# Kernel optimization log

Measured on AMD Instinct MI355X. Metric: run time of the kernel, lower is better.

Reference implementation:

```python
import jax, jax.numpy as jnp
import numpy as np


def setup_inputs() -> dict:
    key = jax.random.key(0)
    k1, k2, k3 = jax.random.split(key, 3)
    N, E, D_IN, D_OUT = 100000, 1600000, 64, 64
    x = jax.random.normal(k1, (N, D_IN), dtype=jnp.float32)
    edge_index = jax.random.randint(k2, (2, E), 0, N, dtype=jnp.int64)
    # Glorot-style init for the GCN weight, zero bias (PyG defaults)
    W = jax.random.normal(k3, (D_IN, D_OUT), dtype=jnp.float32) * (1.0 / np.sqrt(D_IN))
    b = jnp.zeros((D_OUT,), dtype=jnp.float32)
    return {"x": x, "edge_index": edge_index, "W": W, "b": b}


def reference(x, edge_index, W, b):
    # GCNConv (PyG semantics, add_self_loops=True, normalize=True) followed by
    # Dropout (eval mode -> identity) and ReLU.
    N = x.shape[0]
    # Linear transform first (small GEMM)
    xw = x @ W  # [N, D_OUT]
    # Add self-loops
    loops = jnp.arange(N, dtype=edge_index.dtype)
    row = jnp.concatenate([edge_index[0], loops])  # source nodes
    col = jnp.concatenate([edge_index[1], loops])  # destination nodes
    # Symmetric degree normalization: deg over destination index (PyG gcn_norm)
    ones = jnp.ones(col.shape[0], dtype=xw.dtype)
    deg = jax.ops.segment_sum(ones, col, num_segments=N)
    deg_inv_sqrt = jnp.where(deg > 0, jax.lax.rsqrt(deg), 0.0)
    norm = deg_inv_sqrt[row] * deg_inv_sqrt[col]  # [E+N]
    # Gather source features, scale, scatter-add to destinations
    msgs = norm[:, None] * xw[row]  # [E+N, D_OUT]
    out = jax.ops.segment_sum(msgs, col, num_segments=N)
    out = out + b
    # dropout in eval mode is identity
    return jax.nn.relu(out)
```

## Files before the change

### kernel.cpp

```cpp
#include <hip/hip_runtime.h>
#include <hip/hip_fp16.h>


#define D 64
#define BW 256
#define CAP 6144
#define EPT 16
#define PART_T 256
#define EPB (PART_T * EPT)

typedef __attribute__((ext_vector_type(8))) short bf16x8;
typedef __attribute__((ext_vector_type(4))) float f32x4;

__device__ __forceinline__ unsigned short f2bf(float f) {
    unsigned u = __float_as_uint(f);
    u += 0x7FFFu + ((u >> 16) & 1u);
    return (unsigned short)(u >> 16);
}

__global__ void k_part(const int* __restrict__ row, const int* __restrict__ col,
                       int* __restrict__ gcur, int* __restrict__ packed,
                       int E, int NBUCK) {
    extern __shared__ int sh[];
    int* lh   = sh;
    int* base = sh + NBUCK;
    for (int i = threadIdx.x; i < NBUCK; i += PART_T) lh[i] = 0;
    __syncthreads();
    int e0 = blockIdx.x * EPB + threadIdx.x;
    int rr[EPT], cc[EPT], pp[EPT];
#pragma unroll
    for (int i = 0; i < EPT; ++i) {
        int e = e0 + i * PART_T;
        if (e < E) {
            cc[i] = col[e];
            rr[i] = row[e];
            pp[i] = atomicAdd(&lh[cc[i] >> 8], 1);
        } else {
            cc[i] = -1;
        }
    }
    __syncthreads();
    int rot = (int)((blockIdx.x * 97u) % (unsigned)NBUCK);
    for (int j = threadIdx.x; j < NBUCK; j += PART_T) {
        int bu = j + rot; if (bu >= NBUCK) bu -= NBUCK;
        int h = lh[bu];
        if (h > 0) base[bu] = atomicAdd(&gcur[bu * 32], h);
    }
    __syncthreads();
#pragma unroll
    for (int i = 0; i < EPT; ++i) {
        if (cc[i] >= 0) {
            int bu = cc[i] >> 8;
            int pos = base[bu] + pp[i];
            if (pos < CAP)
                packed[(size_t)bu * CAP + pos] = (rr[i] << 8) | (cc[i] & 255);
        }
    }
}

__global__ void k_dis(const int* __restrict__ gcur, const int* __restrict__ packed,
                      float* __restrict__ dis, int N) {
    __shared__ int lh[BW];
    int b = blockIdx.x;
    lh[threadIdx.x] = 0;
    __syncthreads();
    int sz = min(gcur[b * 32], CAP);
    const int* pk = packed + (size_t)b * CAP;
    for (int i = threadIdx.x; i < sz; i += BW)
        atomicAdd(&lh[pk[i] & 255], 1);
    __syncthreads();
    int n = b * BW + threadIdx.x;
    if (n < N) dis[n] = rsqrtf((float)(lh[threadIdx.x] + 1));
}

__global__ __launch_bounds__(256, 4)
void k_gemm_mfma(const float* __restrict__ x, const float* __restrict__ W,
                 const float* __restrict__ dis, unsigned short* __restrict__ xw_h,
                 int N) {
    __shared__ float Ws[64 * 64];
    int tid = threadIdx.x;
    for (int i = tid; i < 4096; i += 256) Ws[i] = W[i];
    __syncthreads();
    int lane = tid & 63, wv = tid >> 6;
    int m = lane & 15, quad = lane >> 4;
    bf16x8 Bf[4][2];
#pragma unroll
    for (int t = 0; t < 4; ++t)
#pragma unroll
        for (int s = 0; s < 2; ++s) {
            bf16x8 f;
#pragma unroll
            for (int j = 0; j < 8; ++j)
                f[j] = (short)f2bf(Ws[(s * 32 + quad * 8 + j) * 64 + t * 16 + m]);
            Bf[t][s] = f;
        }
    int mt = blockIdx.x * 4 + wv;
    int row0 = mt * 16;
    if (row0 >= N) return;
    const float* xr = x + (size_t)(row0 + m) * 64 + quad * 8;
    float4 a0 = *(const float4*)(xr);
    float4 a1 = *(const float4*)(xr + 4);
    float4 a2 = *(const float4*)(xr + 32);
    float4 a3 = *(const float4*)(xr + 36);
    bf16x8 A0, A1;
    A0[0] = (short)f2bf(a0.x); A0[1] = (short)f2bf(a0.y);
    A0[2] = (short)f2bf(a0.z); A0[3] = (short)f2bf(a0.w);
    A0[4] = (short)f2bf(a1.x); A0[5] = (short)f2bf(a1.y);
    A0[6] = (short)f2bf(a1.z); A0[7] = (short)f2bf(a1.w);
    A1[0] = (short)f2bf(a2.x); A1[1] = (short)f2bf(a2.y);
    A1[2] = (short)f2bf(a2.z); A1[3] = (short)f2bf(a2.w);
    A1[4] = (short)f2bf(a3.x); A1[5] = (short)f2bf(a3.y);
    A1[6] = (short)f2bf(a3.z); A1[7] = (short)f2bf(a3.w);
    f32x4 acc[4];
#pragma unroll
    for (int t = 0; t < 4; ++t) {
        acc[t] = (f32x4){0.f, 0.f, 0.f, 0.f};
        acc[t] = __builtin_amdgcn_mfma_f32_16x16x32_bf16(A0, Bf[t][0], acc[t], 0, 0, 0);
        acc[t] = __builtin_amdgcn_mfma_f32_16x16x32_bf16(A1, Bf[t][1], acc[t], 0, 0, 0);
    }
    float4 dv = *(const float4*)(dis + row0 + quad * 4);
    float dsc[4] = {dv.x, dv.y, dv.z, dv.w};
#pragma unroll
    for (int t = 0; t < 4; ++t)
#pragma unroll
        for (int r = 0; r < 4; ++r) {
            int grow = row0 + quad * 4 + r;
            int gcol = t * 16 + m;
            xw_h[(size_t)grow * 64 + gcol] =
                __half_as_ushort(__float2half(acc[t][r] * dsc[r]));
        }
}

__global__ __launch_bounds__(1024, 8)
void k_gather(const int* __restrict__ gcur, const int* __restrict__ packed,
              const uint2* __restrict__ xwh, const float* __restrict__ bias,
              float4* __restrict__ out4, int N) {
    __shared__ int lh[BW], stt[BW], cur[BW];
    __shared__ int srtL[CAP];
    __shared__ int wsum[4];
    int b = blockIdx.x;
    int tid = threadIdx.x;
    if (tid < BW) lh[tid] = 0;
    __syncthreads();
    int sz = min(gcur[b * 32], CAP);
    const int* pk = packed + (size_t)b * CAP;
    for (int i = tid; i < sz; i += 1024)
        atomicAdd(&lh[pk[i] & 255], 1);
    __syncthreads();
    int lane = tid & 63, wv4 = tid >> 6;
    int v = (tid < BW) ? lh[tid] : 0;
    int s = v;
#pragma unroll
    for (int off = 1; off < 64; off <<= 1) {
        int u = __shfl_up(s, off);
        if (lane >= off) s += u;
    }
    if (tid < BW && lane == 63) wsum[wv4] = s;
    __syncthreads();
    if (tid < BW) {
        int woff = 0;
        for (int w = 0; w < 4; ++w) woff += (w < wv4) ? wsum[w] : 0;
        int st = woff + s - v;
        stt[tid] = st;
        cur[tid] = st;
    }
    __syncthreads();
    for (int i = tid; i < sz; i += 1024) {
        int p = pk[i];
        int pos = atomicAdd(&cur[p & 255], 1);
        srtL[pos] = p >> 8;
    }
    __syncthreads();
    int wv = tid >> 6;
    int q = lane >> 4;
    int l = lane & 15;
    const float4 bb = ((const float4*)bias)[l];
#define ADDV(h)                                                     \
    {                                                               \
        __half2 h0 = *(__half2*)&(h).x, h1 = *(__half2*)&(h).y;     \
        float2 f0 = __half22float2(h0), f1 = __half22float2(h1);    \
        acc.x += f0.x; acc.y += f0.y; acc.z += f1.x; acc.w += f1.y; \
    }
    for (int nn = wv * 16; nn < wv * 16 + 16; ++nn) {
        int node = b * BW + nn;
        if (node >= N) break;
        int k = lh[nn], s0 = stt[nn];
        float4 acc = make_float4(0.f, 0.f, 0.f, 0.f);
        if (q == 0) { uint2 hs = xwh[(size_t)node * 16 + l]; ADDV(hs); }
        int j = q;
        for (; j + 12 < k; j += 16) {
            int r0 = srtL[s0 + j];
            int r1 = srtL[s0 + j + 4];
            int r2 = srtL[s0 + j + 8];
            int r3 = srtL[s0 + j + 12];
            uint2 va = xwh[(size_t)r0 * 16 + l];
            uint2 vb = xwh[(size_t)r1 * 16 + l];
            uint2 vc = xwh[(size_t)r2 * 16 + l];
            uint2 vd = xwh[(size_t)r3 * 16 + l];
            ADDV(va); ADDV(vb); ADDV(vc); ADDV(vd);
        }
        for (; j < k; j += 4) { uint2 ve = xwh[(size_t)srtL[s0 + j] * 16 + l]; ADDV(ve); }
#pragma unroll
        for (int mm = 16; mm < 64; mm <<= 1) {
            acc.x += __shfl_xor(acc.x, mm);
            acc.y += __shfl_xor(acc.y, mm);
            acc.z += __shfl_xor(acc.z, mm);
            acc.w += __shfl_xor(acc.w, mm);
        }
        if (q == 0) {
            float dn = rsqrtf((float)(k + 1));
            float4 o;
            o.x = fmaxf(fmaf(dn, acc.x, bb.x), 0.f);
            o.y = fmaxf(fmaf(dn, acc.y, bb.y), 0.f);
            o.z = fmaxf(fmaf(dn, acc.z, bb.z), 0.f);
            o.w = fmaxf(fmaf(dn, acc.w, bb.w), 0.f);
            out4[(size_t)node * 16 + l] = o;
        }
    }
#undef ADDV
}

extern "C" void kernel_launch(void* const* d_in, const int* in_sizes, int n_in,
                              void* d_out, int out_size, void* d_ws, size_t ws_size,
                              hipStream_t stream) {
    const float* x    = (const float*)d_in[0];
    const int*   ei   = (const int*)d_in[1];
    const float* W    = (const float*)d_in[2];
    const float* bias = (const float*)d_in[3];
    float* out = (float*)d_out;

    const int N = in_sizes[0] / D;
    const int E = in_sizes[1] / 2;
    const int* row = ei;
    const int* col = ei + E;

    const int NBUCK = (N + BW - 1) / BW;
    const int NB1   = (E + EPB - 1) / EPB;
    const int NT    = (N + 15) / 16;

    char* ws = (char*)d_ws;
    size_t off = 0;
    unsigned short* xw_h = (unsigned short*)(ws + off); off += (size_t)N * D * sizeof(unsigned short);
    int* packed   = (int*)(ws + off);     off += (size_t)NBUCK * CAP * sizeof(int);
    int* gcur     = (int*)(ws + off);     off += (size_t)NBUCK * 32 * sizeof(int);
    float* dis    = (float*)(ws + off);   off += (size_t)N * sizeof(float);

    size_t ldsPart = 2u * (size_t)NBUCK * sizeof(int);

    hipMemsetAsync(gcur, 0, (size_t)NBUCK * 32 * sizeof(int), stream);
    k_part<<<NB1, PART_T, ldsPart, stream>>>(row, col, gcur, packed, E, NBUCK);
    k_dis<<<NBUCK, BW, 0, stream>>>(gcur, packed, dis, N);
    k_gemm_mfma<<<(NT + 3) / 4, 256, 0, stream>>>(x, W, dis, xw_h, N);
    k_gather<<<NBUCK, 1024, 0, stream>>>(gcur, packed, (const uint2*)xw_h, bias,
                                         (float4*)out, N);
}
```

Before: 160.9 us.

## Fuse partition, degree and gather into one cooperative kernel with grid syncs

Merges the edge partitioning, degree computation and gather-aggregate stages into a single cooperative kernel of 256 persistent blocks separated by grid-wide syncs. Bucket contents are held in registers between phases, which removes the second global read of packed edges. The gcur memset is folded into the GEMM kernel. The source-side normalization moves from the GEMM epilogue into the gather as a per-edge dis lookup, so the GEMM no longer has to wait for degrees. The cost is an extra scattered load per edge, grid.sync overhead, and parallelism fixed at 256 blocks with two buckets each. It also assumes edge and bucket counts fit the fixed per-thread register arrays.

```diff
diff --git a/kernel.cpp b/kernel.cpp
--- a/kernel.cpp
+++ b/kernel.cpp
@@ -1,13 +1,18 @@
 #include <hip/hip_runtime.h>
 #include <hip/hip_fp16.h>
+#include <hip/hip_cooperative_groups.h>
+
+namespace cg = cooperative_groups;
 
 
 #define D 64
 #define BW 256
+#define MAXB 512
 #define CAP 6144
-#define EPT 16
-#define PART_T 256
-#define EPB (PART_T * EPT)
+#define RPT 6
+#define GRID 256
+#define BT 1024
+#define EPT 7
 
 typedef __attribute__((ext_vector_type(8))) short bf16x8;
 typedef __attribute__((ext_vector_type(4))) float f32x4;
@@ -18,65 +23,12 @@
     return (unsigned short)(u >> 16);
 }
 
-__global__ void k_part(const int* __restrict__ row, const int* __restrict__ col,
-                       int* __restrict__ gcur, int* __restrict__ packed,
-                       int E, int NBUCK) {
-    extern __shared__ int sh[];
-    int* lh   = sh;
-    int* base = sh + NBUCK;
-    for (int i = threadIdx.x; i < NBUCK; i += PART_T) lh[i] = 0;
-    __syncthreads();
-    int e0 = blockIdx.x * EPB + threadIdx.x;
-    int rr[EPT], cc[EPT], pp[EPT];
-#pragma unroll
-    for (int i = 0; i < EPT; ++i) {
-        int e = e0 + i * PART_T;
-        if (e < E) {
-            cc[i] = col[e];
-            rr[i] = row[e];
-            pp[i] = atomicAdd(&lh[cc[i] >> 8], 1);
-        } else {
-            cc[i] = -1;
-        }
-    }
-    __syncthreads();
-    int rot = (int)((blockIdx.x * 97u) % (unsigned)NBUCK);
-    for (int j = threadIdx.x; j < NBUCK; j += PART_T) {
-        int bu = j + rot; if (bu >= NBUCK) bu -= NBUCK;
-        int h = lh[bu];
-        if (h > 0) base[bu] = atomicAdd(&gcur[bu * 32], h);
-    }
-    __syncthreads();
-#pragma unroll
-    for (int i = 0; i < EPT; ++i) {
-        if (cc[i] >= 0) {
-            int bu = cc[i] >> 8;
-            int pos = base[bu] + pp[i];
-            if (pos < CAP)
-                packed[(size_t)bu * CAP + pos] = (rr[i] << 8) | (cc[i] & 255);
-        }
-    }
-}
-
-__global__ void k_dis(const int* __restrict__ gcur, const int* __restrict__ packed,
-                      float* __restrict__ dis, int N) {
-    __shared__ int lh[BW];
-    int b = blockIdx.x;
-    lh[threadIdx.x] = 0;
-    __syncthreads();
-    int sz = min(gcur[b * 32], CAP);
-    const int* pk = packed + (size_t)b * CAP;
-    for (int i = threadIdx.x; i < sz; i += BW)
-        atomicAdd(&lh[pk[i] & 255], 1);
-    __syncthreads();
-    int n = b * BW + threadIdx.x;
-    if (n < N) dis[n] = rsqrtf((float)(lh[threadIdx.x] + 1));
-}
-
 __global__ __launch_bounds__(256, 4)
-void k_gemm_mfma(const float* __restrict__ x, const float* __restrict__ W,
-                 const float* __restrict__ dis, unsigned short* __restrict__ xw_h,
-                 int N) {
+void k_gemm(const float* __restrict__ x, const float* __restrict__ W,
+            unsigned short* __restrict__ xw_h, int* __restrict__ zero_base,
+            int nzero, int N) {
+    int zi = blockIdx.x * 256 + threadIdx.x;
+    if (zi < nzero) zero_base[zi] = 0;
     __shared__ float Ws[64 * 64];
     int tid = threadIdx.x;
     for (int i = tid; i < 4096; i += 256) Ws[i] = W[i];
@@ -118,8 +70,6 @@
         acc[t] = __builtin_amdgcn_mfma_f32_16x16x32_bf16(A0, Bf[t][0], acc[t], 0, 0, 0);
         acc[t] = __builtin_amdgcn_mfma_f32_16x16x32_bf16(A1, Bf[t][1], acc[t], 0, 0, 0);
     }
-    float4 dv = *(const float4*)(dis + row0 + quad * 4);
-    float dsc[4] = {dv.x, dv.y, dv.z, dv.w};
 #pragma unroll
     for (int t = 0; t < 4; ++t)
 #pragma unroll
@@ -127,97 +77,172 @@
             int grow = row0 + quad * 4 + r;
             int gcol = t * 16 + m;
             xw_h[(size_t)grow * 64 + gcol] =
-                __half_as_ushort(__float2half(acc[t][r] * dsc[r]));
-        }
-}
-
-__global__ __launch_bounds__(1024, 8)
-void k_gather(const int* __restrict__ gcur, const int* __restrict__ packed,
-              const uint2* __restrict__ xwh, const float* __restrict__ bias,
-              float4* __restrict__ out4, int N) {
-    __shared__ int lh[BW], stt[BW], cur[BW];
+                __half_as_ushort(__float2half(acc[t][r]));
+        }
+}
+
+__global__ __launch_bounds__(BT, 4)
+void k_fused(const int* __restrict__ row, const int* __restrict__ col,
+             int* __restrict__ gcur, int* __restrict__ packed,
+             float* __restrict__ disg, const uint2* __restrict__ xwh,
+             const float* __restrict__ bias, float4* __restrict__ out4,
+             int E, int N, int NBUCK) {
+    __shared__ int lhp[MAXB];
+    __shared__ int basep[MAXB];
+    __shared__ int lhb[2][BW];
+    __shared__ int stt[BW], cur[BW];
+    __shared__ int wsum[4];
     __shared__ int srtL[CAP];
-    __shared__ int wsum[4];
-    int b = blockIdx.x;
+
+    cg::grid_group grid = cg::this_grid();
     int tid = threadIdx.x;
-    if (tid < BW) lh[tid] = 0;
-    __syncthreads();
-    int sz = min(gcur[b * 32], CAP);
-    const int* pk = packed + (size_t)b * CAP;
-    for (int i = tid; i < sz; i += 1024)
-        atomicAdd(&lh[pk[i] & 255], 1);
-    __syncthreads();
-    int lane = tid & 63, wv4 = tid >> 6;
-    int v = (tid < BW) ? lh[tid] : 0;
-    int s = v;
-#pragma unroll
-    for (int off = 1; off < 64; off <<= 1) {
-        int u = __shfl_up(s, off);
-        if (lane >= off) s += u;
-    }
-    if (tid < BW && lane == 63) wsum[wv4] = s;
-    __syncthreads();
-    if (tid < BW) {
-        int woff = 0;
-        for (int w = 0; w < 4; ++w) woff += (w < wv4) ? wsum[w] : 0;
-        int st = woff + s - v;
-        stt[tid] = st;
-        cur[tid] = st;
-    }
-    __syncthreads();
-    for (int i = tid; i < sz; i += 1024) {
-        int p = pk[i];
-        int pos = atomicAdd(&cur[p & 255], 1);
-        srtL[pos] = p >> 8;
-    }
-    __syncthreads();
-    int wv = tid >> 6;
+    int bk  = (int)blockIdx.x;
+
+    for (int i = tid; i < NBUCK; i += BT) lhp[i] = 0;
+    __syncthreads();
+    int epb = (E + GRID - 1) / GRID;
+    int e0 = bk * epb;
+    int eend = min(e0 + epb, E);
+    int rr[EPT], cc[EPT], pp[EPT];
+#pragma unroll
+    for (int i = 0; i < EPT; ++i) {
+        int e = e0 + i * BT + tid;
+        if (e < eend) {
+            cc[i] = col[e]; rr[i] = row[e];
+            pp[i] = atomicAdd(&lhp[cc[i] >> 8], 1);
+        } else cc[i] = -1;
+    }
+    __syncthreads();
+    int rot = (int)((bk * 97u) % (unsigned)NBUCK);
+    for (int j = tid; j < NBUCK; j += BT) {
+        int bu = j + rot; if (bu >= NBUCK) bu -= NBUCK;
+        int h = lhp[bu];
+        if (h > 0) basep[bu] = atomicAdd(&gcur[bu * 32], h);
+    }
+    __syncthreads();
+#pragma unroll
+    for (int i = 0; i < EPT; ++i) {
+        if (cc[i] >= 0) {
+            int bu = cc[i] >> 8;
+            int pos = basep[bu] + pp[i];
+            if (pos < CAP)
+                packed[(size_t)bu * CAP + pos] = (rr[i] << 8) | (cc[i] & 255);
+        }
+    }
+    grid.sync();
+
+    int rv[2][RPT];
+#pragma unroll
+    for (int p = 0; p < 2; ++p) {
+        int b = bk + p * GRID;
+        if (b < NBUCK) {
+            if (tid < BW) lhb[p][tid] = 0;
+            __syncthreads();
+            int sz = min(gcur[b * 32], CAP);
+            const int* pk = packed + (size_t)b * CAP;
+#pragma unroll
+            for (int i = 0; i < RPT; ++i) {
+                int idx = i * BT + tid;
+                int v = (idx < sz) ? pk[idx] : -1;
+                rv[p][i] = v;
+                if (v >= 0) atomicAdd(&lhb[p][v & 255], 1);
+            }
+            __syncthreads();
+            if (tid < BW) {
+                int n = b * BW + tid;
+                if (n < N) disg[n] = rsqrtf((float)(lhb[p][tid] + 1));
+            }
+        }
+    }
+    grid.sync();
+
+    int lane = tid & 63, wv = tid >> 6;
     int q = lane >> 4;
     int l = lane & 15;
     const float4 bb = ((const float4*)bias)[l];
-#define ADDV(h)                                                     \
-    {                                                               \
-        __half2 h0 = *(__half2*)&(h).x, h1 = *(__half2*)&(h).y;     \
-        float2 f0 = __half22float2(h0), f1 = __half22float2(h1);    \
-        acc.x += f0.x; acc.y += f0.y; acc.z += f1.x; acc.w += f1.y; \
-    }
-    for (int nn = wv * 16; nn < wv * 16 + 16; ++nn) {
-        int node = b * BW + nn;
-        if (node >= N) break;
-        int k = lh[nn], s0 = stt[nn];
-        float4 acc = make_float4(0.f, 0.f, 0.f, 0.f);
-        if (q == 0) { uint2 hs = xwh[(size_t)node * 16 + l]; ADDV(hs); }
-        int j = q;
-        for (; j + 12 < k; j += 16) {
-            int r0 = srtL[s0 + j];
-            int r1 = srtL[s0 + j + 4];
-            int r2 = srtL[s0 + j + 8];
-            int r3 = srtL[s0 + j + 12];
-            uint2 va = xwh[(size_t)r0 * 16 + l];
-            uint2 vb = xwh[(size_t)r1 * 16 + l];
-            uint2 vc = xwh[(size_t)r2 * 16 + l];
-            uint2 vd = xwh[(size_t)r3 * 16 + l];
-            ADDV(va); ADDV(vb); ADDV(vc); ADDV(vd);
-        }
-        for (; j < k; j += 4) { uint2 ve = xwh[(size_t)srtL[s0 + j] * 16 + l]; ADDV(ve); }
-#pragma unroll
-        for (int mm = 16; mm < 64; mm <<= 1) {
-            acc.x += __shfl_xor(acc.x, mm);
-            acc.y += __shfl_xor(acc.y, mm);
-            acc.z += __shfl_xor(acc.z, mm);
-            acc.w += __shfl_xor(acc.w, mm);
-        }
-        if (q == 0) {
+#define ADDS(h, ww)                                                         \
+    {                                                                       \
+        __half2 h0 = *(__half2*)&(h).x, h1 = *(__half2*)&(h).y;             \
+        float2 f0 = __half22float2(h0), f1 = __half22float2(h1);            \
+        acc.x = fmaf((ww), f0.x, acc.x); acc.y = fmaf((ww), f0.y, acc.y);   \
+        acc.z = fmaf((ww), f1.x, acc.z); acc.w = fmaf((ww), f1.y, acc.w);   \
+    }
+    for (int p = 0; p < 2; ++p) {
+        int b = bk + p * GRID;
+        if (b >= NBUCK) break;
+        __syncthreads();
+        int v = (tid < BW) ? lhb[p][tid] : 0;
+        int s = v;
+#pragma unroll
+        for (int off = 1; off < 64; off <<= 1) {
+            int u = __shfl_up(s, off);
+            if (lane >= off) s += u;
+        }
+        if (tid < BW && lane == 63) wsum[wv] = s;
+        __syncthreads();
+        if (tid < BW) {
+            int woff = 0;
+            for (int w = 0; w < 4; ++w) woff += (w < wv) ? wsum[w] : 0;
+            int st = woff + s - v;
+            stt[tid] = st; cur[tid] = st;
+        }
+        __syncthreads();
+#pragma unroll
+        for (int i = 0; i < RPT; ++i) {
+            int pv = rv[p][i];
+            if (pv >= 0) {
+                int pos = atomicAdd(&cur[pv & 255], 1);
+                srtL[pos] = pv >> 8;
+            }
+        }
+        __syncthreads();
+        for (int nn = wv * 16; nn < wv * 16 + 16; ++nn) {
+            int node = b * BW + nn;
+            if (node >= N) break;
+            int k = lhb[p][nn], s0 = stt[nn];
             float dn = rsqrtf((float)(k + 1));
-            float4 o;
-            o.x = fmaxf(fmaf(dn, acc.x, bb.x), 0.f);
-            o.y = fmaxf(fmaf(dn, acc.y, bb.y), 0.f);
-            o.z = fmaxf(fmaf(dn, acc.z, bb.z), 0.f);
-            o.w = fmaxf(fmaf(dn, acc.w, bb.w), 0.f);
-            out4[(size_t)node * 16 + l] = o;
-        }
-    }
-#undef ADDV
+            float4 acc = make_float4(0.f, 0.f, 0.f, 0.f);
+            if (q == 0) {
+                uint2 hs = xwh[(size_t)node * 16 + l];
+                ADDS(hs, dn);
+            }
+            int j = q;
+            for (; j + 12 < k; j += 16) {
+                int r0 = srtL[s0 + j];
+                int r1 = srtL[s0 + j + 4];
+                int r2 = srtL[s0 + j + 8];
+                int r3 = srtL[s0 + j + 12];
+                float w0 = disg[r0], w1 = disg[r1], w2 = disg[r2], w3 = disg[r3];
+                uint2 va = xwh[(size_t)r0 * 16 + l];
+                uint2 vb = xwh[(size_t)r1 * 16 + l];
+                uint2 vc = xwh[(size_t)r2 * 16 + l];
+                uint2 vd = xwh[(size_t)r3 * 16 + l];
+                ADDS(va, w0); ADDS(vb, w1); ADDS(vc, w2); ADDS(vd, w3);
+            }
+            for (; j < k; j += 4) {
+                int r = srtL[s0 + j];
+                float wr = disg[r];
+                uint2 ve = xwh[(size_t)r * 16 + l];
+                ADDS(ve, wr);
+            }
+#pragma unroll
+            for (int mm = 16; mm < 64; mm <<= 1) {
+                acc.x += __shfl_xor(acc.x, mm);
+                acc.y += __shfl_xor(acc.y, mm);
+                acc.z += __shfl_xor(acc.z, mm);
+                acc.w += __shfl_xor(acc.w, mm);
+            }
+            if (q == 0) {
+                float4 o;
+                o.x = fmaxf(fmaf(dn, acc.x, bb.x), 0.f);
+                o.y = fmaxf(fmaf(dn, acc.y, bb.y), 0.f);
+                o.z = fmaxf(fmaf(dn, acc.z, bb.z), 0.f);
+                o.w = fmaxf(fmaf(dn, acc.w, bb.w), 0.f);
+                out4[(size_t)node * 16 + l] = o;
+            }
+        }
+    }
+#undef ADDS
 }
 
 extern "C" void kernel_launch(void* const* d_in, const int* in_sizes, int n_in,
@@ -229,28 +254,30 @@
     const float* bias = (const float*)d_in[3];
     float* out = (float*)d_out;
 
-    const int N = in_sizes[0] / D;
-    const int E = in_sizes[1] / 2;
-    const int* row = ei;
-    const int* col = ei + E;
-
-    const int NBUCK = (N + BW - 1) / BW;
-    const int NB1   = (E + EPB - 1) / EPB;
-    const int NT    = (N + 15) / 16;
+    int N = in_sizes[0] / D;
+    int E = in_sizes[1] / 2;
+    const int* rowp = ei;
+    const int* colp = ei + E;
+
+    int NBUCK = (N + BW - 1) / BW;
+    const int NT = (N + 15) / 16;
 
     char* ws = (char*)d_ws;
     size_t off = 0;
-    unsigned short* xw_h = (unsigned short*)(ws + off); off += (size_t)N * D * sizeof(unsigned short);
-    int* packed   = (int*)(ws + off);     off += (size_t)NBUCK * CAP * sizeof(int);
-    int* gcur     = (int*)(ws + off);     off += (size_t)NBUCK * 32 * sizeof(int);
-    float* dis    = (float*)(ws + off);   off += (size_t)N * sizeof(float);
-
-    size_t ldsPart = 2u * (size_t)NBUCK * sizeof(int);
-
-    hipMemsetAsync(gcur, 0, (size_t)NBUCK * 32 * sizeof(int), stream);
-    k_part<<<NB1, PART_T, ldsPart, stream>>>(row, col, gcur, packed, E, NBUCK);
-    k_dis<<<NBUCK, BW, 0, stream>>>(gcur, packed, dis, N);
-    k_gemm_mfma<<<(NT + 3) / 4, 256, 0, stream>>>(x, W, dis, xw_h, N);
-    k_gather<<<NBUCK, 1024, 0, stream>>>(gcur, packed, (const uint2*)xw_h, bias,
-                                         (float4*)out, N);
-}
+    unsigned short* xw_h = (unsigned short*)(ws + off);
+    off += (size_t)N * D * sizeof(unsigned short);
+    int* packed = (int*)(ws + off); off += (size_t)NBUCK * CAP * sizeof(int);
+    int* gcur   = (int*)(ws + off); off += (size_t)NBUCK * 32 * sizeof(int);
+    float* disg = (float*)(ws + off); off += (size_t)N * sizeof(float);
+
+    int nzero = NBUCK * 32;
+
+    k_gemm<<<(NT + 3) / 4, 256, 0, stream>>>(x, W, xw_h, gcur, nzero, N);
+
+    const uint2* xwh_c = (const uint2*)xw_h;
+    float4* outp = (float4*)out;
+    void* args[] = {(void*)&rowp, (void*)&colp, (void*)&gcur, (void*)&packed,
+                    (void*)&disg, (void*)&xwh_c, (void*)&bias, (void*)&outp,
+                    (void*)&E, (void*)&N, (void*)&NBUCK};
+    (void)hipLaunchCooperativeKernel((void*)k_fused, dim3(GRID), dim3(BT), args, 0, stream);
+}
```

New measurement: 261.6 us. 1.63x slower.

## Replace atomic bucket partition with histogram-scan counting sort; move source norm to gather

Applied to the files above, without the earlier changes.

The single-pass partition that grabbed bucket offsets with global atomics into fixed-capacity slabs is replaced by a two-pass counting sort. A per-block bucket histogram is followed by a three-kernel exclusive scan and a scatter into a compact packed array, so bucket ranges are contiguous and deterministic. The GEMM no longer scales rows by the source degree norm and can run first. The gather instead loads the per-source norm for every edge and uses FMAs. This removes global atomic contention and the CAP-strided layout, at the cost of more kernel launches, an extra read of col, and one extra scalar gather per edge.

```diff
diff --git a/kernel.cpp b/kernel.cpp
--- a/kernel.cpp
+++ b/kernel.cpp
@@ -5,9 +5,9 @@
 #define D 64
 #define BW 256
 #define CAP 6144
-#define EPT 16
 #define PART_T 256
-#define EPB (PART_T * EPT)
+#define EPB 4096
+#define SCAN_CHUNK 1024
 
 typedef __attribute__((ext_vector_type(8))) short bf16x8;
 typedef __attribute__((ext_vector_type(4))) float f32x4;
@@ -18,65 +18,9 @@
     return (unsigned short)(u >> 16);
 }
 
-__global__ void k_part(const int* __restrict__ row, const int* __restrict__ col,
-                       int* __restrict__ gcur, int* __restrict__ packed,
-                       int E, int NBUCK) {
-    extern __shared__ int sh[];
-    int* lh   = sh;
-    int* base = sh + NBUCK;
-    for (int i = threadIdx.x; i < NBUCK; i += PART_T) lh[i] = 0;
-    __syncthreads();
-    int e0 = blockIdx.x * EPB + threadIdx.x;
-    int rr[EPT], cc[EPT], pp[EPT];
-#pragma unroll
-    for (int i = 0; i < EPT; ++i) {
-        int e = e0 + i * PART_T;
-        if (e < E) {
-            cc[i] = col[e];
-            rr[i] = row[e];
-            pp[i] = atomicAdd(&lh[cc[i] >> 8], 1);
-        } else {
-            cc[i] = -1;
-        }
-    }
-    __syncthreads();
-    int rot = (int)((blockIdx.x * 97u) % (unsigned)NBUCK);
-    for (int j = threadIdx.x; j < NBUCK; j += PART_T) {
-        int bu = j + rot; if (bu >= NBUCK) bu -= NBUCK;
-        int h = lh[bu];
-        if (h > 0) base[bu] = atomicAdd(&gcur[bu * 32], h);
-    }
-    __syncthreads();
-#pragma unroll
-    for (int i = 0; i < EPT; ++i) {
-        if (cc[i] >= 0) {
-            int bu = cc[i] >> 8;
-            int pos = base[bu] + pp[i];
-            if (pos < CAP)
-                packed[(size_t)bu * CAP + pos] = (rr[i] << 8) | (cc[i] & 255);
-        }
-    }
-}
-
-__global__ void k_dis(const int* __restrict__ gcur, const int* __restrict__ packed,
-                      float* __restrict__ dis, int N) {
-    __shared__ int lh[BW];
-    int b = blockIdx.x;
-    lh[threadIdx.x] = 0;
-    __syncthreads();
-    int sz = min(gcur[b * 32], CAP);
-    const int* pk = packed + (size_t)b * CAP;
-    for (int i = threadIdx.x; i < sz; i += BW)
-        atomicAdd(&lh[pk[i] & 255], 1);
-    __syncthreads();
-    int n = b * BW + threadIdx.x;
-    if (n < N) dis[n] = rsqrtf((float)(lh[threadIdx.x] + 1));
-}
-
 __global__ __launch_bounds__(256, 4)
-void k_gemm_mfma(const float* __restrict__ x, const float* __restrict__ W,
-                 const float* __restrict__ dis, unsigned short* __restrict__ xw_h,
-                 int N) {
+void k_gemm(const float* __restrict__ x, const float* __restrict__ W,
+            unsigned short* __restrict__ xw_h, int N) {
     __shared__ float Ws[64 * 64];
     int tid = threadIdx.x;
     for (int i = tid; i < 4096; i += 256) Ws[i] = W[i];
@@ -94,8 +38,7 @@
                 f[j] = (short)f2bf(Ws[(s * 32 + quad * 8 + j) * 64 + t * 16 + m]);
             Bf[t][s] = f;
         }
-    int mt = blockIdx.x * 4 + wv;
-    int row0 = mt * 16;
+    int row0 = (blockIdx.x * 4 + wv) * 16;
     if (row0 >= N) return;
     const float* xr = x + (size_t)(row0 + m) * 64 + quad * 8;
     float4 a0 = *(const float4*)(xr);
@@ -118,23 +61,131 @@
         acc[t] = __builtin_amdgcn_mfma_f32_16x16x32_bf16(A0, Bf[t][0], acc[t], 0, 0, 0);
         acc[t] = __builtin_amdgcn_mfma_f32_16x16x32_bf16(A1, Bf[t][1], acc[t], 0, 0, 0);
     }
-    float4 dv = *(const float4*)(dis + row0 + quad * 4);
-    float dsc[4] = {dv.x, dv.y, dv.z, dv.w};
 #pragma unroll
     for (int t = 0; t < 4; ++t)
 #pragma unroll
-        for (int r = 0; r < 4; ++r) {
-            int grow = row0 + quad * 4 + r;
-            int gcol = t * 16 + m;
-            xw_h[(size_t)grow * 64 + gcol] =
-                __half_as_ushort(__float2half(acc[t][r] * dsc[r]));
-        }
+        for (int r = 0; r < 4; ++r)
+            xw_h[(size_t)(row0 + quad * 4 + r) * 64 + t * 16 + m] =
+                __half_as_ushort(__float2half(acc[t][r]));
+}
+
+__global__ void k_hist1(const int* __restrict__ col, int* __restrict__ hist,
+                        int E, int NB1, int NBUCK) {
+    extern __shared__ int lhist[];
+    int bk = blockIdx.x;
+    for (int bu = threadIdx.x; bu < NBUCK; bu += PART_T) lhist[bu] = 0;
+    __syncthreads();
+    int base = bk * EPB;
+#pragma unroll 4
+    for (int i = threadIdx.x; i < EPB; i += PART_T) {
+        int e = base + i;
+        if (e < E) atomicAdd(&lhist[col[e] >> 8], 1);
+    }
+    __syncthreads();
+    for (int bu = threadIdx.x; bu < NBUCK; bu += PART_T)
+        hist[bu * NB1 + bk] = lhist[bu];
+}
+
+__global__ void k_blocksum(const int* __restrict__ src, int* __restrict__ partial, int L) {
+    int base = blockIdx.x * SCAN_CHUNK;
+    int s = 0;
+    for (int i = threadIdx.x; i < SCAN_CHUNK; i += 256) {
+        int idx = base + i;
+        s += (idx < L) ? src[idx] : 0;
+    }
+#pragma unroll
+    for (int off = 32; off > 0; off >>= 1) s += __shfl_down(s, off);
+    __shared__ int ws[4];
+    if ((threadIdx.x & 63) == 0) ws[threadIdx.x >> 6] = s;
+    __syncthreads();
+    if (threadIdx.x == 0) partial[blockIdx.x] = ws[0] + ws[1] + ws[2] + ws[3];
+}
+
+__global__ void k_scan_partials(int* __restrict__ partial, int P) {
+    __shared__ int wtot[4];
+    int i = threadIdx.x;
+    int v = (i < P) ? partial[i] : 0;
+    int lane = i & 63, wv = i >> 6;
+    int s = v;
+#pragma unroll
+    for (int off = 1; off < 64; off <<= 1) {
+        int t = __shfl_up(s, off);
+        if (lane >= off) s += t;
+    }
+    if (lane == 63) wtot[wv] = s;
+    __syncthreads();
+    int woff = 0;
+    for (int w = 0; w < 4; ++w) woff += (w < wv) ? wtot[w] : 0;
+    if (i < P) partial[i] = woff + s - v;
+}
+
+__global__ void k_scan_excl(const int* __restrict__ src, const int* __restrict__ partial,
+                            int* __restrict__ dst, int L) {
+    __shared__ int wsum[4];
+    int lane = threadIdx.x & 63, wv = threadIdx.x >> 6;
+    int base = blockIdx.x * SCAN_CHUNK + threadIdx.x * 4;
+    int v0 = (base + 0 < L) ? src[base + 0] : 0;
+    int v1 = (base + 1 < L) ? src[base + 1] : 0;
+    int v2 = (base + 2 < L) ? src[base + 2] : 0;
+    int v3 = (base + 3 < L) ? src[base + 3] : 0;
+    int t = v0 + v1 + v2 + v3;
+    int s = t;
+#pragma unroll
+    for (int off = 1; off < 64; off <<= 1) {
+        int u = __shfl_up(s, off);
+        if (lane >= off) s += u;
+    }
+    if (lane == 63) wsum[wv] = s;
+    __syncthreads();
+    int woff = 0;
+    for (int w = 0; w < 4; ++w) woff += (w < wv) ? wsum[w] : 0;
+    int excl = partial[blockIdx.x] + woff + (s - t);
+    if (base + 0 < L) dst[base + 0] = excl;
+    if (base + 1 < L) dst[base + 1] = excl + v0;
+    if (base + 2 < L) dst[base + 2] = excl + v0 + v1;
+    if (base + 3 < L) dst[base + 3] = excl + v0 + v1 + v2;
+}
+
+__global__ void k_scatter1(const int* __restrict__ row, const int* __restrict__ col,
+                           const int* __restrict__ histS, int* __restrict__ packed,
+                           int E, int NB1, int NBUCK) {
+    extern __shared__ int cur[];
+    int bk = blockIdx.x;
+    for (int bu = threadIdx.x; bu < NBUCK; bu += PART_T)
+        cur[bu] = histS[bu * NB1 + bk];
+    __syncthreads();
+    int base = bk * EPB;
+#pragma unroll 4
+    for (int i = threadIdx.x; i < EPB; i += PART_T) {
+        int e = base + i;
+        if (e < E) {
+            int c = col[e], r = row[e];
+            int pos = atomicAdd(&cur[c >> 8], 1);
+            packed[pos] = (r << 8) | (c & 255);
+        }
+    }
+}
+
+__global__ void k_dis(const int* __restrict__ histS, const int* __restrict__ packed,
+                      float* __restrict__ disg, int E, int NB1, int NBUCK, int N) {
+    __shared__ int lh[BW];
+    int b = blockIdx.x;
+    int lo = histS[b * NB1];
+    int hi = (b == NBUCK - 1) ? E : histS[(b + 1) * NB1];
+    lh[threadIdx.x] = 0;
+    __syncthreads();
+    for (int i = lo + threadIdx.x; i < hi; i += BW)
+        atomicAdd(&lh[packed[i] & 255], 1);
+    __syncthreads();
+    int n = b * BW + threadIdx.x;
+    if (n < N) disg[n] = rsqrtf((float)(lh[threadIdx.x] + 1));
 }
 
 __global__ __launch_bounds__(1024, 8)
-void k_gather(const int* __restrict__ gcur, const int* __restrict__ packed,
-              const uint2* __restrict__ xwh, const float* __restrict__ bias,
-              float4* __restrict__ out4, int N) {
+void k_gather(const int* __restrict__ histS, const int* __restrict__ packed,
+              const float* __restrict__ disg, const uint2* __restrict__ xwh,
+              const float* __restrict__ bias, float4* __restrict__ out4,
+              int E, int NB1, int NBUCK, int N) {
     __shared__ int lh[BW], stt[BW], cur[BW];
     __shared__ int srtL[CAP];
     __shared__ int wsum[4];
@@ -142,8 +193,10 @@
     int tid = threadIdx.x;
     if (tid < BW) lh[tid] = 0;
     __syncthreads();
-    int sz = min(gcur[b * 32], CAP);
-    const int* pk = packed + (size_t)b * CAP;
+    int lo = histS[b * NB1];
+    int hi = (b == NBUCK - 1) ? E : histS[(b + 1) * NB1];
+    int sz = min(hi - lo, CAP);
+    const int* pk = packed + lo;
     for (int i = tid; i < sz; i += 1024)
         atomicAdd(&lh[pk[i] & 255], 1);
     __syncthreads();
@@ -175,31 +228,42 @@
     int q = lane >> 4;
     int l = lane & 15;
     const float4 bb = ((const float4*)bias)[l];
-#define ADDV(h)                                                     \
-    {                                                               \
-        __half2 h0 = *(__half2*)&(h).x, h1 = *(__half2*)&(h).y;     \
-        float2 f0 = __half22float2(h0), f1 = __half22float2(h1);    \
-        acc.x += f0.x; acc.y += f0.y; acc.z += f1.x; acc.w += f1.y; \
+#define ADDS(h, ww)                                                         \
+    {                                                                       \
+        __half2 h0 = *(__half2*)&(h).x, h1 = *(__half2*)&(h).y;             \
+        float2 f0 = __half22float2(h0), f1 = __half22float2(h1);            \
+        acc.x = fmaf((ww), f0.x, acc.x); acc.y = fmaf((ww), f0.y, acc.y);   \
+        acc.z = fmaf((ww), f1.x, acc.z); acc.w = fmaf((ww), f1.y, acc.w);   \
     }
     for (int nn = wv * 16; nn < wv * 16 + 16; ++nn) {
         int node = b * BW + nn;
         if (node >= N) break;
         int k = lh[nn], s0 = stt[nn];
+        float dn = rsqrtf((float)(k + 1));
         float4 acc = make_float4(0.f, 0.f, 0.f, 0.f);
-        if (q == 0) { uint2 hs = xwh[(size_t)node * 16 + l]; ADDV(hs); }
+        if (q == 0) {
+            uint2 hs = xwh[(size_t)node * 16 + l];
+            ADDS(hs, dn);
+        }
         int j = q;
         for (; j + 12 < k; j += 16) {
             int r0 = srtL[s0 + j];
             int r1 = srtL[s0 + j + 4];
             int r2 = srtL[s0 + j + 8];
             int r3 = srtL[s0 + j + 12];
+            float w0 = disg[r0], w1 = disg[r1], w2 = disg[r2], w3 = disg[r3];
             uint2 va = xwh[(size_t)r0 * 16 + l];
             uint2 vb = xwh[(size_t)r1 * 16 + l];
             uint2 vc = xwh[(size_t)r2 * 16 + l];
             uint2 vd = xwh[(size_t)r3 * 16 + l];
-            ADDV(va); ADDV(vb); ADDV(vc); ADDV(vd);
-        }
-        for (; j < k; j += 4) { uint2 ve = xwh[(size_t)srtL[s0 + j] * 16 + l]; ADDV(ve); }
+            ADDS(va, w0); ADDS(vb, w1); ADDS(vc, w2); ADDS(vd, w3);
+        }
+        for (; j < k; j += 4) {
+            int r = srtL[s0 + j];
+            float wr = disg[r];
+            uint2 ve = xwh[(size_t)r * 16 + l];
+            ADDS(ve, wr);
+        }
 #pragma unroll
         for (int mm = 16; mm < 64; mm <<= 1) {
             acc.x += __shfl_xor(acc.x, mm);
@@ -208,7 +272,6 @@
             acc.w += __shfl_xor(acc.w, mm);
         }
         if (q == 0) {
-            float dn = rsqrtf((float)(k + 1));
             float4 o;
             o.x = fmaxf(fmaf(dn, acc.x, bb.x), 0.f);
             o.y = fmaxf(fmaf(dn, acc.y, bb.y), 0.f);
@@ -217,7 +280,7 @@
             out4[(size_t)node * 16 + l] = o;
         }
     }
-#undef ADDV
+#undef ADDS
 }
 
 extern "C" void kernel_launch(void* const* d_in, const int* in_sizes, int n_in,
@@ -236,21 +299,29 @@
 
     const int NBUCK = (N + BW - 1) / BW;
     const int NB1   = (E + EPB - 1) / EPB;
+    const int L     = NBUCK * NB1;
+    const int P     = (L + SCAN_CHUNK - 1) / SCAN_CHUNK;
     const int NT    = (N + 15) / 16;
 
     char* ws = (char*)d_ws;
     size_t off = 0;
-    unsigned short* xw_h = (unsigned short*)(ws + off); off += (size_t)N * D * sizeof(unsigned short);
-    int* packed   = (int*)(ws + off);     off += (size_t)NBUCK * CAP * sizeof(int);
-    int* gcur     = (int*)(ws + off);     off += (size_t)NBUCK * 32 * sizeof(int);
-    float* dis    = (float*)(ws + off);   off += (size_t)N * sizeof(float);
-
-    size_t ldsPart = 2u * (size_t)NBUCK * sizeof(int);
-
-    hipMemsetAsync(gcur, 0, (size_t)NBUCK * 32 * sizeof(int), stream);
-    k_part<<<NB1, PART_T, ldsPart, stream>>>(row, col, gcur, packed, E, NBUCK);
-    k_dis<<<NBUCK, BW, 0, stream>>>(gcur, packed, dis, N);
-    k_gemm_mfma<<<(NT + 3) / 4, 256, 0, stream>>>(x, W, dis, xw_h, N);
-    k_gather<<<NBUCK, 1024, 0, stream>>>(gcur, packed, (const uint2*)xw_h, bias,
-                                         (float4*)out, N);
-}
+    unsigned short* xw_h = (unsigned short*)(ws + off);
+    off += (size_t)N * D * sizeof(unsigned short);
+    int*   packed  = (int*)(ws + off);   off += (size_t)E * sizeof(int);
+    int*   hist    = (int*)(ws + off);   off += (size_t)L * sizeof(int);
+    int*   histS   = (int*)(ws + off);   off += (size_t)L * sizeof(int);
+    float* disg    = (float*)(ws + off); off += (size_t)N * sizeof(float);
+    int*   partial = (int*)(ws + off);   off += 256 * sizeof(int);
+
+    size_t lds1 = (size_t)NBUCK * sizeof(int);
+
+    k_gemm<<<(NT + 3) / 4, 256, 0, stream>>>(x, W, xw_h, N);
+    k_hist1<<<NB1, PART_T, lds1, stream>>>(col, hist, E, NB1, NBUCK);
+    k_blocksum<<<P, 256, 0, stream>>>(hist, partial, L);
+    k_scan_partials<<<1, 256, 0, stream>>>(partial, P);
+    k_scan_excl<<<P, 256, 0, stream>>>(hist, partial, histS, L);
+    k_scatter1<<<NB1, PART_T, lds1, stream>>>(row, col, histS, packed, E, NB1, NBUCK);
+    k_dis<<<NBUCK, BW, 0, stream>>>(histS, packed, disg, E, NB1, NBUCK, N);
+    k_gather<<<NBUCK, 1024, 0, stream>>>(histS, packed, disg, (const uint2*)xw_h,
+                                         bias, (float4*)out, E, NB1, NBUCK, N);
+}
```

Result: slower. 175.4 us (+9.1%).
